# Performance work log

Measured on AMD Instinct MI355X. Metric: run time of the kernel, lower is better.

## Reference

```python
import jax, jax.numpy as jnp
import numpy as np

DIM, HEADS = 1536, 12
HD = DIM // HEADS            # 128 head dim
C = HD // 2                  # 64 complex (pair) dim
C0 = C - 2 * (C // 3)        # 22 (temporal axis)
C1 = C // 3                  # 21 (each spatial axis)
MAX_POS = 1024
F_, H_, W_ = 9, 22, 22
SEQ = F_ * H_ * W_           # 4356
NCLASS = 2
EPS = 1e-6


def _rope_tables():
    # Wan rope_params: theta = 10000, per-axis half-dims C0, C1, C1.
    def ang(half):
        inv = 1.0 / (10000.0 ** (np.arange(0, 2 * half, 2) / (2 * half)))
        return np.outer(np.arange(MAX_POS), inv)
    a = np.concatenate([ang(C0), ang(C1), ang(C1)], axis=1)  # [MAX_POS, C]
    return jnp.asarray(np.cos(a), jnp.float32), jnp.asarray(np.sin(a), jnp.float32)


def setup_inputs() -> dict:
    key = jax.random.key(0)
    ks = jax.random.split(key, 6)
    s = 1.0 / np.sqrt(DIM)
    def lin(k):
        k1, k2 = jax.random.split(k)
        return (jax.random.uniform(k1, (DIM, DIM), jnp.float32, -s, s),
                jax.random.uniform(k2, (DIM,), jnp.float32, -s, s))
    Wq, bq = lin(ks[0]); Wk, bk = lin(ks[1]); Wv, bv = lin(ks[2]); Wo, bo = lin(ks[3])
    fc, fs = _rope_tables()
    masks = (jax.random.uniform(ks[4], (NCLASS, H_ * W_)) < 0.5).astype(jnp.float32)
    x = jax.random.normal(ks[5], (1, SEQ, DIM), jnp.float32)
    return {"x": x, "Wq": Wq, "bq": bq, "Wk": Wk, "bk": bk, "Wv": Wv, "bv": bv,
            "Wo": Wo, "bo": bo, "gq": jnp.ones((DIM,), jnp.float32),
            "gk": jnp.ones((DIM,), jnp.float32), "freqs_cos": fc, "freqs_sin": fs,
            "ref_target_masks": masks, "f": F_, "h": H_, "w": W_}


def _rmsnorm(x, g):
    return x * jax.lax.rsqrt(jnp.mean(x * x, axis=-1, keepdims=True) + EPS) * g


def _grid_cs(tab, f, h, w):
    # per-position (f,h,w) rope table -> [f*h*w, C]
    p0 = jnp.broadcast_to(tab[:f, None, None, :C0], (f, h, w, C0))
    p1 = jnp.broadcast_to(tab[None, :h, None, C0:C0 + C1], (f, h, w, C1))
    p2 = jnp.broadcast_to(tab[None, None, :w, C0 + C1:], (f, h, w, C1))
    return jnp.concatenate([p0, p1, p2], axis=-1).reshape(f * h * w, C)


def _rope(x, cos, sin):
    # x: [b,s,n,d]; pairs are interleaved along d (view_as_complex semantics)
    b, s, n, d = x.shape
    xr = x.reshape(b, s, n, d // 2, 2)
    a, bi = xr[..., 0], xr[..., 1]
    cos = cos[None, :, None, :]
    sin = sin[None, :, None, :]
    out = jnp.stack([a * cos - bi * sin, a * sin + bi * cos], axis=-1)
    return out.reshape(b, s, n, d)


def reference(x, Wq, bq, Wk, bk, Wv, bv, Wo, bo, gq, gk, freqs_cos, freqs_sin,
              ref_target_masks, f, h, w):
    b, s, _ = x.shape
    n, d = HEADS, HD
    q = _rmsnorm(x @ Wq.T + bq, gq).reshape(b, s, n, d)
    k = _rmsnorm(x @ Wk.T + bk, gk).reshape(b, s, n, d)
    v = (x @ Wv.T + bv).reshape(b, s, n, d)
    cos = _grid_cs(freqs_cos, f, h, w)
    sin = _grid_cs(freqs_sin, f, h, w)
    q = _rope(q, cos, sin)
    k = _rope(k, cos, sin)
    scale = 1.0 / np.sqrt(d).astype(np.float32)
    # full (window_size == (-1,-1)) attention; seq_lens == s so k_lens mask is identity
    scores = jnp.einsum('bsnd,btnd->bnst', q, k) * scale
    p = jax.nn.softmax(scores, axis=-1)
    o = jnp.einsum('bnst,btnd->bsnd', p, v).reshape(b, s, n * d)
    out = o @ Wo.T + bo
    # aux attention map vs reference-frame keys (first h*w spatial tokens), no-grad path
    xs = h * w
    ref_k = k[:, :xs]
    s2 = jnp.einsum('bsnd,btnd->bnst', q * scale, ref_k)
    p2 = jax.nn.softmax(s2, axis=-1)                       # [b,n,s,xs]
    m = ref_target_masks                                   # [c,xs]
    maps = jnp.einsum('bnst,ct->cbns', p2, m) / jnp.sum(m, axis=-1)[:, None, None, None]
    attn_map = maps.mean(axis=2).reshape(-1, s)            # mean over heads -> [c*b, s]
    return out, attn_map
```

## Files before the change

kernel.cpp:

```cpp
#include <hip/hip_runtime.h>
#include <hip/hip_bf16.h>
#include <math.h>

constexpr int SEQ   = 4356;
constexpr int DIM   = 1536;
constexpr int HEADS = 12;
constexpr int HD    = 128;
constexpr int CH    = 64;
constexpr int C0c   = 22;
constexpr int C1c   = 21;
constexpr int WWc   = 22;
constexpr int HHWW  = 484;
constexpr int XS    = 484;
constexpr int KVB   = 32;
constexpr int NT    = (SEQ + KVB - 1) / KVB;
constexpr int SEQP  = 4416;
constexpr size_t SD = (size_t)SEQ * DIM;

typedef float f32x4 __attribute__((ext_vector_type(4)));
typedef short bf16x8 __attribute__((ext_vector_type(8)));
typedef short bf16x4 __attribute__((ext_vector_type(4)));

__device__ inline unsigned short f2bf(float f) {
  union { float f; unsigned u; } x; x.f = f;
  return (unsigned short)((x.u + 0x7FFFu + ((x.u >> 16) & 1u)) >> 16);
}
__device__ inline float bf2f(unsigned short u) {
  union { unsigned u; float f; } x; x.u = ((unsigned)u) << 16;
  return x.f;
}

#define GLD16(g, l)                                                                        \
  __builtin_amdgcn_global_load_lds((const __attribute__((address_space(1))) unsigned*)    \
                                       (const void*)(g),                                  \
                                   (__attribute__((address_space(3))) unsigned*)(void*)(l),\
                                   16, 0, 0)

__global__ __launch_bounds__(256) void prep_kernel(const float* __restrict__ mask,
                                                   float* __restrict__ cnt,
                                                   float4* __restrict__ msk4) {
  int t = threadIdx.x;
  for (int i = t; i < 512; i += 256) {
    float4 v;
    v.x = (i < XS) ? mask[i] : 0.f;
    v.y = (i < XS) ? mask[XS + i] : 0.f;
    v.z = (i < XS) ? 1.f : 0.f;
    v.w = 0.f;
    msk4[i] = v;
  }
  float c0 = 0.f, c1 = 0.f;
  for (int i = t; i < XS; i += 256) { c0 += mask[i]; c1 += mask[XS + i]; }
  __shared__ float red0[256];
  __shared__ float red1[256];
  red0[t] = c0; red1[t] = c1;
  __syncthreads();
  for (int off = 128; off > 0; off >>= 1) {
    if (t < off) { red0[t] += red0[t + off]; red1[t] += red1[t + off]; }
    __syncthreads();
  }
  if (t == 0) { cnt[0] = red0[0]; cnt[1] = red1[0]; }
}

__global__ __launch_bounds__(256) void padzero(unsigned short* __restrict__ vt,
                                               float* __restrict__ amap) {
  const int gid = blockIdx.x * 256 + threadIdx.x;
  const int stride = gridDim.x * 256;
  for (int i = gid; i < 2 * SEQ; i += stride) amap[i] = 0.f;
  const int pad = SEQP - SEQ;
  const int total = DIM * pad;
  for (int i = gid; i < total; i += stride) {
    const int d = i / pad, c = i - d * pad;
    vt[(size_t)d * SEQP + SEQ + c] = 0;
  }
}

__global__ __launch_bounds__(256) void to_bf16(const float* __restrict__ in,
                                               unsigned short* __restrict__ out, int n4) {
  for (int i = blockIdx.x * 256 + threadIdx.x; i < n4; i += gridDim.x * 256) {
    const float4 v = ((const float4*)in)[i];
    ushort4 o;
    o.x = f2bf(v.x); o.y = f2bf(v.y); o.z = f2bf(v.z); o.w = f2bf(v.w);
    ((ushort4*)out)[i] = o;
  }
}

__global__ __launch_bounds__(256) void to_bf16_w(const float* __restrict__ W0, const float* __restrict__ W1,
                                                 const float* __restrict__ W2, const float* __restrict__ W3,
                                                 unsigned short* __restrict__ o0, unsigned short* __restrict__ o1,
                                                 unsigned short* __restrict__ o2, unsigned short* __restrict__ o3,
                                                 int n4) {
  const int z = blockIdx.z;
  const float* in = (z == 0) ? W0 : (z == 1) ? W1 : (z == 2) ? W2 : W3;
  unsigned short* out = (z == 0) ? o0 : (z == 1) ? o1 : (z == 2) ? o2 : o3;
  for (int i = blockIdx.x * 256 + threadIdx.x; i < n4; i += gridDim.x * 256) {
    const float4 v = ((const float4*)in)[i];
    ushort4 o;
    o.x = f2bf(v.x); o.y = f2bf(v.y); o.z = f2bf(v.z); o.w = f2bf(v.w);
    ((ushort4*)out)[i] = o;
  }
}

__global__ __launch_bounds__(256) void gemm_qkv(const unsigned short* __restrict__ A,
                                                const unsigned short* __restrict__ B0,
                                                const unsigned short* __restrict__ B1,
                                                const unsigned short* __restrict__ B2,
                                                const float* __restrict__ bq,
                                                const float* __restrict__ bk,
                                                const float* __restrict__ bv,
                                                unsigned short* __restrict__ o0,
                                                unsigned short* __restrict__ o1,
                                                unsigned short* __restrict__ vtout,
                                                int M) {
  __shared__ unsigned short As[128 * 64];
  __shared__ unsigned short Bs[128 * 64];
  const int z = blockIdx.z;
  const unsigned short* B = (z == 0) ? B0 : (z == 1) ? B1 : B2;
  const float* bias = (z == 0) ? bq : (z == 1) ? bk : bv;
  const int t    = threadIdx.x;
  const int lane = t & 63;
  const int w    = t >> 6;
  const int wr   = w >> 1, wc = w & 1;
  const int bm = blockIdx.x * 128, bn = blockIdx.y * 128;
  const int lq = lane & 15, lg = lane >> 4;
  f32x4 acc[4][4] = {};
  for (int k0 = 0; k0 < DIM; k0 += 64) {
#pragma unroll
    for (int i = 0; i < 4; ++i) {
      const int idx = i * 256 + t;
      const int row = idx >> 3;
      const int c8  = (idx & 7) * 8;
      const int ga  = min(bm + row, M - 1);
      GLD16(A + (size_t)ga * DIM + k0 + c8, As + idx * 8);
      const int gb  = bn + row;
      GLD16(B + (size_t)gb * DIM + k0 + c8, Bs + idx * 8);
    }
    __syncthreads();
#pragma unroll
    for (int kk = 0; kk < 2; ++kk) {
      bf16x8 af[4], bf[4];
#pragma unroll
      for (int m = 0; m < 4; ++m)
        af[m] = *(const bf16x8*)(As + (wr * 64 + m * 16 + lq) * 64 + kk * 32 + lg * 8);
#pragma unroll
      for (int n = 0; n < 4; ++n)
        bf[n] = *(const bf16x8*)(Bs + (wc * 64 + n * 16 + lq) * 64 + kk * 32 + lg * 8);
#pragma unroll
      for (int m = 0; m < 4; ++m)
#pragma unroll
        for (int n = 0; n < 4; ++n)
          acc[m][n] = __builtin_amdgcn_mfma_f32_16x16x32_bf16(af[m], bf[n], acc[m][n], 0, 0, 0);
    }
    __syncthreads();
  }
#pragma unroll
  for (int n = 0; n < 4; ++n) {
    const int col = bn + wc * 64 + n * 16 + lq;
    const float bv2 = bias[col];
#pragma unroll
    for (int m = 0; m < 4; ++m) {
      const int rm = bm + wr * 64 + m * 16 + lg * 4;
      if (z < 2) {
        unsigned short* C = (z == 0) ? o0 : o1;
#pragma unroll
        for (int r = 0; r < 4; ++r) {
          const int row = rm + r;
          if (row < M) C[(size_t)row * DIM + col] = f2bf(acc[m][n][r] + bv2);
        }
      } else {
        if (rm < M) {
          bf16x4 o;
#pragma unroll
          for (int r = 0; r < 4; ++r) o[r] = (short)f2bf(acc[m][n][r] + bv2);
          *(bf16x4*)(vtout + (size_t)col * SEQP + rm) = o;
        }
      }
    }
  }
}

__global__ __launch_bounds__(256) void gemm_mfma(const unsigned short* __restrict__ A,
                                                 const unsigned short* __restrict__ B,
                                                 const float* __restrict__ bias,
                                                 float* __restrict__ C, int M) {
  __shared__ unsigned short As[128 * 64];
  __shared__ unsigned short Bs[128 * 64];
  const int t    = threadIdx.x;
  const int lane = t & 63;
  const int w    = t >> 6;
  const int wr   = w >> 1, wc = w & 1;
  const int bm = blockIdx.x * 128, bn = blockIdx.y * 128;
  const int lq = lane & 15, lg = lane >> 4;
  f32x4 acc[4][4] = {};
  for (int k0 = 0; k0 < DIM; k0 += 64) {
#pragma unroll
    for (int i = 0; i < 4; ++i) {
      const int idx = i * 256 + t;
      const int row = idx >> 3;
      const int c8  = (idx & 7) * 8;
      const int ga  = min(bm + row, M - 1);
      GLD16(A + (size_t)ga * DIM + k0 + c8, As + idx * 8);
      const int gb  = bn + row;
      GLD16(B + (size_t)gb * DIM + k0 + c8, Bs + idx * 8);
    }
    __syncthreads();
#pragma unroll
    for (int kk = 0; kk < 2; ++kk) {
      bf16x8 af[4], bf[4];
#pragma unroll
      for (int m = 0; m < 4; ++m)
        af[m] = *(const bf16x8*)(As + (wr * 64 + m * 16 + lq) * 64 + kk * 32 + lg * 8);
#pragma unroll
      for (int n = 0; n < 4; ++n)
        bf[n] = *(const bf16x8*)(Bs + (wc * 64 + n * 16 + lq) * 64 + kk * 32 + lg * 8);
#pragma unroll
      for (int m = 0; m < 4; ++m)
#pragma unroll
        for (int n = 0; n < 4; ++n)
          acc[m][n] = __builtin_amdgcn_mfma_f32_16x16x32_bf16(af[m], bf[n], acc[m][n], 0, 0, 0);
    }
    __syncthreads();
  }
#pragma unroll
  for (int n = 0; n < 4; ++n) {
    const int col = bn + wc * 64 + n * 16 + lq;
    const float bv = bias[col];
#pragma unroll
    for (int m = 0; m < 4; ++m) {
      const int rm = bm + wr * 64 + m * 16 + lg * 4;
#pragma unroll
      for (int r = 0; r < 4; ++r) {
        const int row = rm + r;
        if (row < M) C[(size_t)row * DIM + col] = acc[m][n][r] + bv;
      }
    }
  }
}

__global__ __launch_bounds__(256) void rms_rope2(unsigned short* __restrict__ qb,
                                                 unsigned short* __restrict__ kb,
                                                 const float* __restrict__ gq,
                                                 const float* __restrict__ gk,
                                                 const float* __restrict__ fcos,
                                                 const float* __restrict__ fsin) {
  const int z = blockIdx.y;
  unsigned short* row = (z ? kb : qb) + (size_t)blockIdx.x * DIM;
  const float* g = z ? gk : gq;
  const float scale = z ? 1.0f : 0.08838834764831845f;
  const int s = blockIdx.x;
  const int t = threadIdx.x;
  float ss = 0.f;
  for (int i = t; i < DIM / 8; i += 256) {
    const bf16x8 v = ((const bf16x8*)row)[i];
#pragma unroll
    for (int j = 0; j < 8; ++j) {
      const float f = bf2f((unsigned short)v[j]);
      ss = fmaf(f, f, ss);
    }
  }
#pragma unroll
  for (int off = 1; off < 64; off <<= 1) ss += __shfl_xor(ss, off);
  __shared__ float wred[4];
  if ((t & 63) == 0) wred[t >> 6] = ss;
  __syncthreads();
  const float tot = wred[0] + wred[1] + wred[2] + wred[3];
  const float rs = rsqrtf(tot * (1.0f / DIM) + 1e-6f);
  const int fi  = s / HHWW;
  const int rem = s - fi * HHWW;
  const int hi  = rem / WWc;
  const int wi  = rem - hi * WWc;
  for (int p = t; p < DIM / 2; p += 256) {
    const int head = p >> 6;
    const int c    = p & 63;
    const int idx  = head * HD + 2 * c;
    const int trow = (c < C0c) ? fi : ((c < C0c + C1c) ? hi : wi);
    const float co = fcos[trow * CH + c];
    const float si = fsin[trow * CH + c];
    const ushort2 in = *(const ushort2*)(row + idx);
    const float a  = bf2f(in.x) * rs * g[idx];
    const float b  = bf2f(in.y) * rs * g[idx + 1];
    ushort2 pr;
    pr.x = f2bf((a * co - b * si) * scale);
    pr.y = f2bf((a * si + b * co) * scale);
    *(ushort2*)(row + idx) = pr;
  }
}

#define SOFT_QS(QS, SACC, MAP_, LAST_, KBV)                                                \
  {                                                                                        \
    float sv[8];                                                                           \
    _Pragma("unroll")                                                                      \
    for (int i = 0; i < 8; ++i) {                                                          \
      float v = SACC[i >> 2][i & 3];                                                       \
      if (LAST_) { const int key = (KBV) + (i >> 2) * 16 + lg * 4 + (i & 3);               \
                   if (key >= SEQ) v = -1e30f; }                                           \
      sv[i] = __expf(v);                                                                   \
      ls[QS] += sv[i];                                                                     \
    }                                                                                      \
    if (MAP_) {                                                                            \
      _Pragma("unroll")                                                                    \
      for (int i = 0; i < 8; ++i) {                                                        \
        const int key = (KBV) + (i >> 2) * 16 + lg * 4 + (i & 3);                          \
        const float4 mv = msk4[key];                                                       \
        n0[QS] = fmaf(sv[i], mv.x, n0[QS]);                                                \
        n1[QS] = fmaf(sv[i], mv.y, n1[QS]);                                                \
        d2[QS] = fmaf(sv[i], mv.z, d2[QS]);                                                \
      }                                                                                    \
    }                                                                                      \
    _Pragma("unroll")                                                                      \
    for (int kbi = 0; kbi < 2; ++kbi) {                                                    \
      unsigned r0, r1;                                                                     \
      asm("v_cvt_pk_bf16_f32 %0, %1, %2" : "=v"(r0) : "v"(sv[kbi*4+0]), "v"(sv[kbi*4+1])); \
      asm("v_cvt_pk_bf16_f32 %0, %1, %2" : "=v"(r1) : "v"(sv[kbi*4+2]), "v"(sv[kbi*4+3])); \
      uint2 pw; pw.x = r0; pw.y = r1;                                                      \
      *(uint2*)&Pw[QS][lq][kbi * 16 + lg * 4] = pw;                                        \
    }                                                                                      \
  }

#define TILE_BODY(KB_, MAP_, LAST_, PRE_, W0_)                                             \
  {                                                                                        \
    const int kb_ = (KB_);                                                                 \
    const int tt_ = kb_ >> 5;                                                              \
    const unsigned short* Kc = Ks[tt_ % 3];                                                \
    const unsigned short* Vc = Vs[tt_ % 3];                                                \
    if (W0_) { asm volatile("s_waitcnt vmcnt(0)" ::: "memory"); }                          \
    else     { asm volatile("s_waitcnt vmcnt(4)" ::: "memory"); }                          \
    __builtin_amdgcn_s_barrier();                                                          \
    __builtin_amdgcn_sched_barrier(0);                                                     \
    if (PRE_) {                                                                            \
      const int pb_ = (tt_ + 2) % 3;                                                       \
      unsigned short* Kn = Ks[pb_];                                                        \
      unsigned short* Vn = Vs[pb_];                                                        \
      const int kbn = kb_ + 2 * KVB;                                                       \
      _Pragma("unroll")                                                                    \
      for (int j = 0; j < 2; ++j) {                                                        \
        const int ck = t + j * 256;                                                        \
        const int kr = ck >> 4, ksl = ck & 15;                                             \
        GLD16(kh + (size_t)min(kbn + kr, SEQ - 1) * DIM + ((ksl ^ (kr & 7)) * 8),          \
              Kn + ck * 8);                                                                \
        const int vd = ck >> 2, vsl = ck & 3;                                              \
        GLD16(vh + (size_t)vd * SEQP + kbn + ((vsl ^ ((vd >> 1) & 3)) * 8),                \
              Vn + ck * 8);                                                                \
      }                                                                                    \
    }                                                                                      \
    f32x4 sacc0[2] = {}, sacc1[2] = {};                                                    \
    __builtin_amdgcn_s_setprio(1);                                                         \
    _Pragma("unroll")                                                                      \
    for (int kbi = 0; kbi < 2; ++kbi) {                                                    \
      const int krow = kbi * 16 + lq;                                                      \
      _Pragma("unroll")                                                                    \
      for (int c = 0; c < 4; ++c) {                                                        \
        const bf16x8 kf = *(const bf16x8*)(Kc + (krow * 16 + ((c * 4 + lg) ^ (krow & 7))) * 8); \
        sacc0[kbi] = __builtin_amdgcn_mfma_f32_16x16x32_bf16(kf, qf0[c], sacc0[kbi], 0, 0, 0);  \
        sacc1[kbi] = __builtin_amdgcn_mfma_f32_16x16x32_bf16(kf, qf1[c], sacc1[kbi], 0, 0, 0);  \
      }                                                                                    \
    }                                                                                      \
    __builtin_amdgcn_s_setprio(0);                                                         \
    SOFT_QS(0, sacc0, MAP_, LAST_, kb_)                                                    \
    SOFT_QS(1, sacc1, MAP_, LAST_, kb_)                                                    \
    {                                                                                      \
      const bf16x8 pf0 = *(const bf16x8*)&Pw[0][lq][lg * 8];                               \
      const bf16x8 pf1 = *(const bf16x8*)&Pw[1][lq][lg * 8];                               \
      __builtin_amdgcn_s_setprio(1);                                                       \
      _Pragma("unroll")                                                                    \
      for (int db = 0; db < 8; ++db) {                                                     \
        const int vd = db * 16 + lq;                                                       \
        const bf16x8 vf = *(const bf16x8*)(Vc + (vd * 4 + (lg ^ ((vd >> 1) & 3))) * 8);    \
        acc0[db] = __builtin_amdgcn_mfma_f32_16x16x32_bf16(vf, pf0, acc0[db], 0, 0, 0);    \
        acc1[db] = __builtin_amdgcn_mfma_f32_16x16x32_bf16(vf, pf1, acc1[db], 0, 0, 0);    \
      }                                                                                    \
      __builtin_amdgcn_s_setprio(0);                                                       \
    }                                                                                      \
  }

__global__ __launch_bounds__(256, 2) void flash_mfma(const unsigned short* __restrict__ qbuf,
                                                     const unsigned short* __restrict__ kbuf,
                                                     const unsigned short* __restrict__ vt,
                                                     const float4* __restrict__ msk4,
                                                     const float* __restrict__ cnt,
                                                     unsigned short* __restrict__ ob,
                                                     float* __restrict__ amap) {
  const int h    = blockIdx.y;
  const int t    = threadIdx.x;
  const int w    = t >> 6;
  const int lane = t & 63;
  const int lq   = lane & 15, lg = lane >> 4;
  const int qbase = blockIdx.x * 128 + w * 32;

  __shared__ __align__(16) unsigned short Ks[3][KVB * 128];
  __shared__ __align__(16) unsigned short Vs[3][128 * KVB];
  __shared__ __align__(16) unsigned short Plds[4][2][16][40];
  unsigned short (*Pw)[16][40] = Plds[w];

  const unsigned short* kh = kbuf + h * HD;
  const unsigned short* vh = vt + (size_t)(h * HD) * SEQP;

  const int qsrc0 = min(qbase + lq, SEQ - 1);
  const int qsrc1 = min(qbase + 16 + lq, SEQ - 1);
  bf16x8 qf0[4], qf1[4];
#pragma unroll
  for (int c = 0; c < 4; ++c) {
    qf0[c] = *(const bf16x8*)(qbuf + (size_t)qsrc0 * DIM + h * HD + c * 32 + lg * 8);
    qf1[c] = *(const bf16x8*)(qbuf + (size_t)qsrc1 * DIM + h * HD + c * 32 + lg * 8);
  }

  f32x4 acc0[8] = {}, acc1[8] = {};
  float ls[2] = {0.f, 0.f};
  float d2[2] = {0.f, 0.f}, n0[2] = {0.f, 0.f}, n1[2] = {0.f, 0.f};

#pragma unroll
  for (int j = 0; j < 2; ++j) {
    const int ck = t + j * 256;
    const int kr = ck >> 4, ksl = ck & 15;
    GLD16(kh + (size_t)min(kr, SEQ - 1) * DIM + ((ksl ^ (kr & 7)) * 8), Ks[0] + ck * 8);
    const int vd = ck >> 2, vsl = ck & 3;
    GLD16(vh + (size_t)vd * SEQP + ((vsl ^ ((vd >> 1) & 3)) * 8), Vs[0] + ck * 8);
  }
#pragma unroll
  for (int j = 0; j < 2; ++j) {
    const int ck = t + j * 256;
    const int kr = ck >> 4, ksl = ck & 15;
    GLD16(kh + (size_t)min(KVB + kr, SEQ - 1) * DIM + ((ksl ^ (kr & 7)) * 8), Ks[1] + ck * 8);
    const int vd = ck >> 2, vsl = ck & 3;
    GLD16(vh + (size_t)vd * SEQP + KVB + ((vsl ^ ((vd >> 1) & 3)) * 8), Vs[1] + ck * 8);
  }

  for (int tile = 0; tile < 16; ++tile)         TILE_BODY(tile * KVB, true,  false, true,  false);
  for (int tile = 16; tile < NT - 2; ++tile)    TILE_BODY(tile * KVB, false, false, true,  false);
  TILE_BODY((NT - 2) * KVB, false, false, false, false);
  TILE_BODY((NT - 1) * KVB, false, true,  false, true);

#pragma unroll
  for (int qs = 0; qs < 2; ++qs) {
    ls[qs] += __shfl_xor(ls[qs], 16);
    ls[qs] += __shfl_xor(ls[qs], 32);
  }
  {
    const int qrow = qbase + lq;
    if (qrow < SEQ) {
      const float inv = 1.f / ls[0];
#pragma unroll
      for (int db = 0; db < 8; ++db) {
        bf16x4 o;
#pragma unroll
        for (int r = 0; r < 4; ++r) o[r] = (short)f2bf(acc0[db][r] * inv);
        *(bf16x4*)(ob + (size_t)qrow * DIM + h * HD + db * 16 + lg * 4) = o;
      }
    }
  }
  {
    const int qrow = qbase + 16 + lq;
    if (qrow < SEQ) {
      const float inv = 1.f / ls[1];
#pragma unroll
      for (int db = 0; db < 8; ++db) {
        bf16x4 o;
#pragma unroll
        for (int r = 0; r < 4; ++r) o[r] = (short)f2bf(acc1[db][r] * inv);
        *(bf16x4*)(ob + (size_t)qrow * DIM + h * HD + db * 16 + lg * 4) = o;
      }
    }
  }
#pragma unroll
  for (int qs = 0; qs < 2; ++qs) {
    float dd = d2[qs], a0 = n0[qs], a1 = n1[qs];
    dd += __shfl_xor(dd, 16); dd += __shfl_xor(dd, 32);
    a0 += __shfl_xor(a0, 16); a0 += __shfl_xor(a0, 32);
    a1 += __shfl_xor(a1, 16); a1 += __shfl_xor(a1, 32);
    const int qrow = qbase + qs * 16 + lq;
    if (lane < 16 && qrow < SEQ) {
      const float invd = 1.f / (dd * (float)HEADS);
      atomicAdd(&amap[qrow],       a0 * invd / cnt[0]);
      atomicAdd(&amap[SEQ + qrow], a1 * invd / cnt[1]);
    }
  }
}

extern "C" void kernel_launch(void* const* d_in, const int* in_sizes, int n_in,
                              void* d_out, int out_size, void* d_ws, size_t ws_size,
                              hipStream_t stream) {
  const float* x    = (const float*)d_in[0];
  const float* Wq   = (const float*)d_in[1];
  const float* bq   = (const float*)d_in[2];
  const float* Wk   = (const float*)d_in[3];
  const float* bk   = (const float*)d_in[4];
  const float* Wv   = (const float*)d_in[5];
  const float* bv   = (const float*)d_in[6];
  const float* Wo   = (const float*)d_in[7];
  const float* bo   = (const float*)d_in[8];
  const float* gq   = (const float*)d_in[9];
  const float* gk   = (const float*)d_in[10];
  const float* fc   = (const float*)d_in[11];
  const float* fs   = (const float*)d_in[12];
  const float* mask = (const float*)d_in[13];

  float* out  = (float*)d_out;
  float* amap = out + SD;

  float* f32b        = (float*)d_ws;
  unsigned short* xb = (unsigned short*)(f32b + SD);
  unsigned short* qb = xb + SD;
  unsigned short* kb = qb + SD;
  unsigned short* vt = kb + SD;
  unsigned short* wqb = vt + (size_t)DIM * SEQP;
  unsigned short* wkb = wqb + (size_t)DIM * DIM;
  unsigned short* wvb = wkb + (size_t)DIM * DIM;
  unsigned short* wob = wvb + (size_t)DIM * DIM;
  float4* msk4 = (float4*)(wob + (size_t)DIM * DIM);
  float* cnt  = (float*)(msk4 + 512);
  unsigned short* ob = (unsigned short*)f32b;

  prep_kernel<<<1, 256, 0, stream>>>(mask, cnt, msk4);
  padzero<<<64, 256, 0, stream>>>(vt, amap);
  to_bf16<<<2048, 256, 0, stream>>>(x, xb, (int)(SD / 4));
  constexpr int W4 = DIM * DIM / 4;
  to_bf16_w<<<dim3(512, 1, 4), 256, 0, stream>>>(Wq, Wk, Wv, Wo, wqb, wkb, wvb, wob, W4);

  const dim3 gg((SEQ + 127) / 128, DIM / 128, 3);
  gemm_qkv<<<gg, 256, 0, stream>>>(xb, wqb, wkb, wvb, bq, bk, bv, qb, kb, vt, SEQ);

  rms_rope2<<<dim3(SEQ, 2), 256, 0, stream>>>(qb, kb, gq, gk, fc, fs);

  const dim3 fg((SEQ + 127) / 128, HEADS);
  flash_mfma<<<fg, 256, 0, stream>>>(qb, kb, vt, msk4, cnt, ob, amap);

  const dim3 go((SEQ + 127) / 128, DIM / 128);
  gemm_mfma<<<go, 256, 0, stream>>>(ob, wob, bo, out, SEQ);
}
```

Baseline: 397.1 us.

## Software-pipeline QK^T MFMA one tile ahead of softmax in flash attention

The K/V tile loop is restructured so the QK^T MFMAs for tile t+1 are issued before the softmax and PV step of tile t. Two score-accumulator register sets alternate between iterations, and a prologue and an explicit tail tile are added. The goal is to hide the exp/softmax VALU work and LDS P-writes behind matrix-core work, keeping the MFMA pipe busy. The cost is extra score registers, which could hurt occupancy or cause spills at 2 waves per SIMD, plus a changed order of waitcnt and barriers.

```diff
diff --git a/kernel.cpp b/kernel.cpp
--- a/kernel.cpp
+++ b/kernel.cpp
@@ -316,18 +316,31 @@
     }                                                                                      \
   }
 
-#define TILE_BODY(KB_, MAP_, LAST_, PRE_, W0_)                                             \
+#define S_MFMA(TN_, SC0, SC1)                                                              \
   {                                                                                        \
-    const int kb_ = (KB_);                                                                 \
-    const int tt_ = kb_ >> 5;                                                              \
-    const unsigned short* Kc = Ks[tt_ % 3];                                                \
-    const unsigned short* Vc = Vs[tt_ % 3];                                                \
-    if (W0_) { asm volatile("s_waitcnt vmcnt(0)" ::: "memory"); }                          \
-    else     { asm volatile("s_waitcnt vmcnt(4)" ::: "memory"); }                          \
+    const unsigned short* Kc_ = Ks[(TN_) % 3];                                             \
+    SC0[0] = z4; SC0[1] = z4; SC1[0] = z4; SC1[1] = z4;                                    \
+    __builtin_amdgcn_s_setprio(1);                                                         \
+    _Pragma("unroll")                                                                      \
+    for (int kbi = 0; kbi < 2; ++kbi) {                                                    \
+      const int krow = kbi * 16 + lq;                                                      \
+      _Pragma("unroll")                                                                    \
+      for (int c = 0; c < 4; ++c) {                                                        \
+        const bf16x8 kf = *(const bf16x8*)(Kc_ + (krow * 16 + ((c * 4 + lg) ^ (krow & 7))) * 8); \
+        SC0[kbi] = __builtin_amdgcn_mfma_f32_16x16x32_bf16(kf, qf0[c], SC0[kbi], 0, 0, 0); \
+        SC1[kbi] = __builtin_amdgcn_mfma_f32_16x16x32_bf16(kf, qf1[c], SC1[kbi], 0, 0, 0); \
+      }                                                                                    \
+    }                                                                                      \
+    __builtin_amdgcn_s_setprio(0);                                                         \
+  }
+
+#define TILE_PIPE(T_, MAP_, PRE_, W0_, SP0, SP1, SC0, SC1)                                 \
+  {                                                                                        \
+    const int t_  = (T_);                                                                  \
+    const int kb_ = t_ * KVB;                                                              \
     __builtin_amdgcn_s_barrier();                                                          \
-    __builtin_amdgcn_sched_barrier(0);                                                     \
     if (PRE_) {                                                                            \
-      const int pb_ = (tt_ + 2) % 3;                                                       \
+      const int pb_ = (t_ + 2) % 3;                                                        \
       unsigned short* Kn = Ks[pb_];                                                        \
       unsigned short* Vn = Vs[pb_];                                                        \
       const int kbn = kb_ + 2 * KVB;                                                       \
@@ -342,22 +355,15 @@
               Vn + ck * 8);                                                                \
       }                                                                                    \
     }                                                                                      \
-    f32x4 sacc0[2] = {}, sacc1[2] = {};                                                    \
-    __builtin_amdgcn_s_setprio(1);                                                         \
-    _Pragma("unroll")                                                                      \
-    for (int kbi = 0; kbi < 2; ++kbi) {                                                    \
-      const int krow = kbi * 16 + lq;                                                      \
-      _Pragma("unroll")                                                                    \
-      for (int c = 0; c < 4; ++c) {                                                        \
-        const bf16x8 kf = *(const bf16x8*)(Kc + (krow * 16 + ((c * 4 + lg) ^ (krow & 7))) * 8); \
-        sacc0[kbi] = __builtin_amdgcn_mfma_f32_16x16x32_bf16(kf, qf0[c], sacc0[kbi], 0, 0, 0);  \
-        sacc1[kbi] = __builtin_amdgcn_mfma_f32_16x16x32_bf16(kf, qf1[c], sacc1[kbi], 0, 0, 0);  \
-      }                                                                                    \
-    }                                                                                      \
-    __builtin_amdgcn_s_setprio(0);                                                         \
-    SOFT_QS(0, sacc0, MAP_, LAST_, kb_)                                                    \
-    SOFT_QS(1, sacc1, MAP_, LAST_, kb_)                                                    \
+    __builtin_amdgcn_sched_barrier(0);                                                     \
+    if (W0_) { asm volatile("s_waitcnt vmcnt(0)" ::: "memory"); }                          \
+    else     { asm volatile("s_waitcnt vmcnt(4)" ::: "memory"); }                          \
+    __builtin_amdgcn_sched_barrier(0);                                                     \
+    S_MFMA(t_ + 1, SC0, SC1)                                                               \
+    SOFT_QS(0, SP0, MAP_, false, kb_)                                                      \
+    SOFT_QS(1, SP1, MAP_, false, kb_)                                                      \
     {                                                                                      \
+      const unsigned short* Vc = Vs[t_ % 3];                                               \
       const bf16x8 pf0 = *(const bf16x8*)&Pw[0][lq][lg * 8];                               \
       const bf16x8 pf1 = *(const bf16x8*)&Pw[1][lq][lg * 8];                               \
       __builtin_amdgcn_s_setprio(1);                                                       \
@@ -394,6 +400,8 @@
   const unsigned short* kh = kbuf + h * HD;
   const unsigned short* vh = vt + (size_t)(h * HD) * SEQP;
 
+  const f32x4 z4 = {0.f, 0.f, 0.f, 0.f};
+
   const int qsrc0 = min(qbase + lq, SEQ - 1);
   const int qsrc1 = min(qbase + 16 + lq, SEQ - 1);
   bf16x8 qf0[4], qf1[4];
@@ -404,6 +412,7 @@
   }
 
   f32x4 acc0[8] = {}, acc1[8] = {};
+  f32x4 sA0[2], sA1[2], sB0[2], sB1[2];
   float ls[2] = {0.f, 0.f};
   float d2[2] = {0.f, 0.f}, n0[2] = {0.f, 0.f}, n1[2] = {0.f, 0.f};
 
@@ -423,11 +432,36 @@
     const int vd = ck >> 2, vsl = ck & 3;
     GLD16(vh + (size_t)vd * SEQP + KVB + ((vsl ^ ((vd >> 1) & 3)) * 8), Vs[1] + ck * 8);
   }
-
-  for (int tile = 0; tile < 16; ++tile)         TILE_BODY(tile * KVB, true,  false, true,  false);
-  for (int tile = 16; tile < NT - 2; ++tile)    TILE_BODY(tile * KVB, false, false, true,  false);
-  TILE_BODY((NT - 2) * KVB, false, false, false, false);
-  TILE_BODY((NT - 1) * KVB, false, true,  false, true);
+  asm volatile("s_waitcnt vmcnt(4)" ::: "memory");
+  __builtin_amdgcn_s_barrier();
+  S_MFMA(0, sA0, sA1)
+
+  for (int tt = 0; tt < 16; tt += 2) {
+    TILE_PIPE(tt,     true,  true, false, sA0, sA1, sB0, sB1)
+    TILE_PIPE(tt + 1, true,  true, false, sB0, sB1, sA0, sA1)
+  }
+  for (int tt = 16; tt < 134; tt += 2) {
+    TILE_PIPE(tt,     false, true, false, sA0, sA1, sB0, sB1)
+    TILE_PIPE(tt + 1, false, true, false, sB0, sB1, sA0, sA1)
+  }
+  TILE_PIPE(134, false, true,  false, sA0, sA1, sB0, sB1)
+  TILE_PIPE(135, false, false, true,  sB0, sB1, sA0, sA1)
+  {
+    const int kb_ = 136 * KVB;
+    __builtin_amdgcn_s_barrier();
+    SOFT_QS(0, sA0, false, true, kb_)
+    SOFT_QS(1, sA1, false, true, kb_)
+    const unsigned short* Vc = Vs[136 % 3];
+    const bf16x8 pf0 = *(const bf16x8*)&Pw[0][lq][lg * 8];
+    const bf16x8 pf1 = *(const bf16x8*)&Pw[1][lq][lg * 8];
+#pragma unroll
+    for (int db = 0; db < 8; ++db) {
+      const int vd = db * 16 + lq;
+      const bf16x8 vf = *(const bf16x8*)(Vc + (vd * 4 + (lg ^ ((vd >> 1) & 3))) * 8);
+      acc0[db] = __builtin_amdgcn_mfma_f32_16x16x32_bf16(vf, pf0, acc0[db], 0, 0, 0);
+      acc1[db] = __builtin_amdgcn_mfma_f32_16x16x32_bf16(vf, pf1, acc1[db], 0, 0, 0);
+    }
+  }
 
 #pragma unroll
   for (int qs = 0; qs < 2; ++qs) {
```

Result: faster. 388.2 us, median of 2 (-2.2%).
